# Kernel optimization log

Measured on AMD Instinct MI355X. Metric: run time of the kernel, lower is better.

Reference implementation:

```python
import jax, jax.numpy as jnp
import numpy as np

EPS = 1e-8  # torch CosineSimilarity eps


def setup_inputs() -> dict:
    key = jax.random.key(0)
    ks = jax.random.split(key, 7)
    N, D, H = 8192, 3, 256
    return {
        "pattern1": jax.random.normal(ks[0], (D,), jnp.float32),
        "pattern2": jax.random.normal(ks[1], (D,), jnp.float32),
        "working_memory": jax.random.normal(ks[2], (N, D), jnp.float32),
        "Wp": jax.random.normal(ks[3], (H, D), jnp.float32) * 0.1,
        "bp": jax.random.normal(ks[4], (H,), jnp.float32) * 0.1,
        "Wq": jax.random.normal(ks[5], (H, D), jnp.float32) * 0.1,
        "bq": jax.random.normal(ks[6], (H,), jnp.float32) * 0.1,
    }


def reference(pattern1, pattern2, working_memory, Wp, bp, Wq, bq):
    # Embed patterns and all propositions (torch Linear: x @ W.T + b)
    p1 = pattern1 @ Wp.T + bp                       # (H,)
    p2 = pattern2 @ Wp.T + bp                       # (H,)
    props = working_memory @ Wq.T + bq              # (N, H)
    prop_norm = jnp.linalg.norm(props, axis=-1)     # (N,)

    def match(pemb):
        # sigmoid(cosine_sim(pemb, props))  -> (N,)
        num = props @ pemb
        den = jnp.maximum(prop_norm * jnp.linalg.norm(pemb), EPS)
        return jax.nn.sigmoid(num / den)

    m1 = match(p1)                                  # (N,)
    m2 = match(p2)                                  # (N,)

    # Entity-link: cosine sim of scalar wm[i,2] with wm[j,0]
    obj = working_memory[:, 2]                      # (N,)
    subj = working_memory[:, 0]                     # (N,)
    num = obj[:, None] * subj[None, :]              # (N, N)
    den = jnp.maximum(jnp.abs(obj)[:, None] * jnp.abs(subj)[None, :], EPS)
    link = jax.nn.sigmoid(num / den)                # (N, N)

    out = m1[:, None] * m2[None, :] * link          # (N, N)
    N = out.shape[0]
    # zero the diagonal (i != j in the original loop)
    return out * (1.0 - jnp.eye(N, dtype=out.dtype))
```

## Files before the change

kernel.cpp:

```cpp
#include <hip/hip_runtime.h>
#include <math.h>

#define EPS 1e-8f
constexpr int N = 8192;
constexpr int ROWS_PER_BLOCK = 16;
constexpr int COLS_PER_BLOCK = 1024;
constexpr float LPOS = 0.7310585786300049f;
constexpr float LNEG = 0.2689414213699951f;

__global__ __launch_bounds__(256) void match_kernel(
    const float* __restrict__ pat1, const float* __restrict__ pat2,
    const float* __restrict__ Wp, const float* __restrict__ bp,
    const float* __restrict__ wm, const float* __restrict__ Wq,
    const float* __restrict__ bq,
    float4* __restrict__ rowpack, float* __restrict__ m2,
    float* __restrict__ subj) {
  const int row = (blockIdx.x * blockDim.x + threadIdx.x) >> 6;
  const int lane = threadIdx.x & 63;
  const float a0 = pat1[0], a1 = pat1[1], a2 = pat1[2];
  const float b0 = pat2[0], b1 = pat2[1], b2 = pat2[2];
  const float x0 = wm[row * 3 + 0];
  const float x1 = wm[row * 3 + 1];
  const float x2 = wm[row * 3 + 2];
  float s0 = 0.f, s1 = 0.f, s2 = 0.f, n1 = 0.f, n2 = 0.f;
#pragma unroll
  for (int k = 0; k < 4; ++k) {
    const int h = lane + k * 64;
    const float wp0 = Wp[h * 3 + 0], wp1 = Wp[h * 3 + 1], wp2 = Wp[h * 3 + 2];
    const float bph = bp[h];
    const float v1 = fmaf(wp0, a0, fmaf(wp1, a1, fmaf(wp2, a2, bph)));
    const float v2 = fmaf(wp0, b0, fmaf(wp1, b1, fmaf(wp2, b2, bph)));
    const float v  = fmaf(Wq[h * 3 + 0], x0,
                     fmaf(Wq[h * 3 + 1], x1,
                     fmaf(Wq[h * 3 + 2], x2, bq[h])));
    s0 = fmaf(v, v, s0);
    s1 = fmaf(v, v1, s1);
    s2 = fmaf(v, v2, s2);
    n1 = fmaf(v1, v1, n1);
    n2 = fmaf(v2, v2, n2);
  }
#pragma unroll
  for (int off = 32; off > 0; off >>= 1) {
    s0 += __shfl_xor(s0, off, 64);
    s1 += __shfl_xor(s1, off, 64);
    s2 += __shfl_xor(s2, off, 64);
    n1 += __shfl_xor(n1, off, 64);
    n2 += __shfl_xor(n2, off, 64);
  }
  if (lane == 0) {
    const float pn = sqrtf(s0);
    const float d1 = fmaxf(pn * sqrtf(n1), EPS);
    const float d2 = fmaxf(pn * sqrtf(n2), EPS);
    const float mm1 = 1.f / (1.f + __expf(-(s1 / d1)));
    const float mm2 = 1.f / (1.f + __expf(-(s2 / d2)));
    m2[row]   = mm2;
    subj[row] = x0;
    float4 rp;
    rp.x = mm1;
    rp.y = x2;
    rp.z = EPS / fabsf(x2);
    rp.w = 0.f;
    rowpack[row] = rp;
  }
}

__device__ __forceinline__ float exact_elem(float a, float oi, float m2c,
                                            float sjc) {
  const float t = oi * sjc;
  const float z = t / fmaxf(fabsf(t), EPS);
  return a * m2c * (1.f / (1.f + __expf(-z)));
}

template <bool DIAG>
__device__ __forceinline__ void run_rows(
    const float4* __restrict__ rowpack, int iBase, int jBase,
    float4 m2v, float4 sjv, float4 qp, float4 qm, float4 asj, float minasj,
    float* __restrict__ out) {
#pragma unroll
  for (int r = 0; r < ROWS_PER_BLOCK; ++r) {
    const int i = iBase + r;
    const float4 rp = rowpack[i];
    const float a = rp.x, oi = rp.y, thr = rp.z;
    const bool neg = oi < 0.f;
    float4 o;
    o.x = a * (neg ? qm.x : qp.x);
    o.y = a * (neg ? qm.y : qp.y);
    o.z = a * (neg ? qm.z : qp.z);
    o.w = a * (neg ? qm.w : qp.w);
    if (__builtin_expect(__any(minasj < thr), 0)) {
      if (asj.x < thr) o.x = exact_elem(a, oi, m2v.x, sjv.x);
      if (asj.y < thr) o.y = exact_elem(a, oi, m2v.y, sjv.y);
      if (asj.z < thr) o.z = exact_elem(a, oi, m2v.z, sjv.z);
      if (asj.w < thr) o.w = exact_elem(a, oi, m2v.w, sjv.w);
    }
    if (DIAG) {
      if (jBase + 0 == i) o.x = 0.f;
      if (jBase + 1 == i) o.y = 0.f;
      if (jBase + 2 == i) o.z = 0.f;
      if (jBase + 3 == i) o.w = 0.f;
    }
    *reinterpret_cast<float4*>(out + (size_t)i * N + jBase) = o;
  }
}

__global__ __launch_bounds__(256) void outer_kernel(
    const float4* __restrict__ rowpack, const float* __restrict__ m2,
    const float* __restrict__ subj, float* __restrict__ out) {
  const int jBase = blockIdx.x * COLS_PER_BLOCK + threadIdx.x * 4;
  const int iBase = blockIdx.y * ROWS_PER_BLOCK;
  const float4 m2v = *reinterpret_cast<const float4*>(m2 + jBase);
  const float4 sjv = *reinterpret_cast<const float4*>(subj + jBase);
  float4 qp, qm, asj;
  qp.x = m2v.x * (sjv.x > 0.f ? LPOS : LNEG);
  qp.y = m2v.y * (sjv.y > 0.f ? LPOS : LNEG);
  qp.z = m2v.z * (sjv.z > 0.f ? LPOS : LNEG);
  qp.w = m2v.w * (sjv.w > 0.f ? LPOS : LNEG);
  qm.x = m2v.x * (sjv.x > 0.f ? LNEG : LPOS);
  qm.y = m2v.y * (sjv.y > 0.f ? LNEG : LPOS);
  qm.z = m2v.z * (sjv.z > 0.f ? LNEG : LPOS);
  qm.w = m2v.w * (sjv.w > 0.f ? LNEG : LPOS);
  asj.x = fabsf(sjv.x);
  asj.y = fabsf(sjv.y);
  asj.z = fabsf(sjv.z);
  asj.w = fabsf(sjv.w);
  const float minasj = fminf(fminf(asj.x, asj.y), fminf(asj.z, asj.w));
  if ((iBase >> 10) == (int)blockIdx.x)
    run_rows<true>(rowpack, iBase, jBase, m2v, sjv, qp, qm, asj, minasj, out);
  else
    run_rows<false>(rowpack, iBase, jBase, m2v, sjv, qp, qm, asj, minasj, out);
}

extern "C" void kernel_launch(void* const* d_in, const int* in_sizes, int n_in,
                              void* d_out, int out_size, void* d_ws,
                              size_t ws_size, hipStream_t stream) {
  const float* pat1 = (const float*)d_in[0];
  const float* pat2 = (const float*)d_in[1];
  const float* wm   = (const float*)d_in[2];
  const float* Wp   = (const float*)d_in[3];
  const float* bp   = (const float*)d_in[4];
  const float* Wq   = (const float*)d_in[5];
  const float* bq   = (const float*)d_in[6];
  float* out = (float*)d_out;

  float4* rowpack = (float4*)d_ws;
  float* m2   = (float*)(rowpack + N);
  float* subj = m2 + N;

  match_kernel<<<N / 4, 256, 0, stream>>>(pat1, pat2, Wp, bp, wm, Wq, bq,
                                          rowpack, m2, subj);
  dim3 grid(N / COLS_PER_BLOCK, N / ROWS_PER_BLOCK);
  outer_kernel<<<grid, 256, 0, stream>>>(rowpack, m2, subj, out);
}
```

Measured before the change: 50.45 us.

## Make outer kernel persistent over row tiles with software-prefetched rowpack

Shrinks the outer-product grid from 8x512 to 8x64 blocks, so each block loops over 8 row tiles. It reuses the per-column setup (m2, subj, qp/qm) across all of its tiles. The rowpack entries for the next tile are prefetched into registers while the current tile is stored. This cuts per-block launch and setup overhead and hides rowpack load latency, but it raises register pressure and leaves fewer blocks in flight to saturate the store bandwidth of a 256MB write.

```diff
diff --git a/kernel.cpp b/kernel.cpp
--- a/kernel.cpp
+++ b/kernel.cpp
@@ -5,6 +5,8 @@
 constexpr int N = 8192;
 constexpr int ROWS_PER_BLOCK = 16;
 constexpr int COLS_PER_BLOCK = 1024;
+constexpr int NTILES = N / ROWS_PER_BLOCK;
+constexpr int YBLOCKS = 64;
 constexpr float LPOS = 0.7310585786300049f;
 constexpr float LNEG = 0.2689414213699951f;
 
@@ -71,43 +73,11 @@
   return a * m2c * (1.f / (1.f + __expf(-z)));
 }
 
-template <bool DIAG>
-__device__ __forceinline__ void run_rows(
-    const float4* __restrict__ rowpack, int iBase, int jBase,
-    float4 m2v, float4 sjv, float4 qp, float4 qm, float4 asj, float minasj,
-    float* __restrict__ out) {
-#pragma unroll
-  for (int r = 0; r < ROWS_PER_BLOCK; ++r) {
-    const int i = iBase + r;
-    const float4 rp = rowpack[i];
-    const float a = rp.x, oi = rp.y, thr = rp.z;
-    const bool neg = oi < 0.f;
-    float4 o;
-    o.x = a * (neg ? qm.x : qp.x);
-    o.y = a * (neg ? qm.y : qp.y);
-    o.z = a * (neg ? qm.z : qp.z);
-    o.w = a * (neg ? qm.w : qp.w);
-    if (__builtin_expect(__any(minasj < thr), 0)) {
-      if (asj.x < thr) o.x = exact_elem(a, oi, m2v.x, sjv.x);
-      if (asj.y < thr) o.y = exact_elem(a, oi, m2v.y, sjv.y);
-      if (asj.z < thr) o.z = exact_elem(a, oi, m2v.z, sjv.z);
-      if (asj.w < thr) o.w = exact_elem(a, oi, m2v.w, sjv.w);
-    }
-    if (DIAG) {
-      if (jBase + 0 == i) o.x = 0.f;
-      if (jBase + 1 == i) o.y = 0.f;
-      if (jBase + 2 == i) o.z = 0.f;
-      if (jBase + 3 == i) o.w = 0.f;
-    }
-    *reinterpret_cast<float4*>(out + (size_t)i * N + jBase) = o;
-  }
-}
-
 __global__ __launch_bounds__(256) void outer_kernel(
     const float4* __restrict__ rowpack, const float* __restrict__ m2,
     const float* __restrict__ subj, float* __restrict__ out) {
-  const int jBase = blockIdx.x * COLS_PER_BLOCK + threadIdx.x * 4;
-  const int iBase = blockIdx.y * ROWS_PER_BLOCK;
+  const int bx = blockIdx.x;
+  const int jBase = bx * COLS_PER_BLOCK + threadIdx.x * 4;
   const float4 m2v = *reinterpret_cast<const float4*>(m2 + jBase);
   const float4 sjv = *reinterpret_cast<const float4*>(subj + jBase);
   float4 qp, qm, asj;
@@ -124,10 +94,51 @@
   asj.z = fabsf(sjv.z);
   asj.w = fabsf(sjv.w);
   const float minasj = fminf(fminf(asj.x, asj.y), fminf(asj.z, asj.w));
-  if ((iBase >> 10) == (int)blockIdx.x)
-    run_rows<true>(rowpack, iBase, jBase, m2v, sjv, qp, qm, asj, minasj, out);
-  else
-    run_rows<false>(rowpack, iBase, jBase, m2v, sjv, qp, qm, asj, minasj, out);
+
+  int by = blockIdx.y;
+  float4 rp[ROWS_PER_BLOCK];
+#pragma unroll
+  for (int r = 0; r < ROWS_PER_BLOCK; ++r)
+    rp[r] = rowpack[by * ROWS_PER_BLOCK + r];
+
+  while (by < NTILES) {
+    const int nby = by + YBLOCKS;
+    float4 rpn[ROWS_PER_BLOCK];
+    if (nby < NTILES) {
+#pragma unroll
+      for (int r = 0; r < ROWS_PER_BLOCK; ++r)
+        rpn[r] = rowpack[nby * ROWS_PER_BLOCK + r];
+    }
+    const int iBase = by * ROWS_PER_BLOCK;
+    const bool diagTile = (iBase >> 10) == bx;
+#pragma unroll
+    for (int r = 0; r < ROWS_PER_BLOCK; ++r) {
+      const int i = iBase + r;
+      const float a = rp[r].x, oi = rp[r].y, thr = rp[r].z;
+      const bool neg = oi < 0.f;
+      float4 o;
+      o.x = a * (neg ? qm.x : qp.x);
+      o.y = a * (neg ? qm.y : qp.y);
+      o.z = a * (neg ? qm.z : qp.z);
+      o.w = a * (neg ? qm.w : qp.w);
+      if (__builtin_expect(__any(minasj < thr), 0)) {
+        if (asj.x < thr) o.x = exact_elem(a, oi, m2v.x, sjv.x);
+        if (asj.y < thr) o.y = exact_elem(a, oi, m2v.y, sjv.y);
+        if (asj.z < thr) o.z = exact_elem(a, oi, m2v.z, sjv.z);
+        if (asj.w < thr) o.w = exact_elem(a, oi, m2v.w, sjv.w);
+      }
+      if (diagTile) {
+        if (jBase + 0 == i) o.x = 0.f;
+        if (jBase + 1 == i) o.y = 0.f;
+        if (jBase + 2 == i) o.z = 0.f;
+        if (jBase + 3 == i) o.w = 0.f;
+      }
+      *reinterpret_cast<float4*>(out + (size_t)i * N + jBase) = o;
+    }
+#pragma unroll
+    for (int r = 0; r < ROWS_PER_BLOCK; ++r) rp[r] = rpn[r];
+    by = nby;
+  }
 }
 
 extern "C" void kernel_launch(void* const* d_in, const int* in_sizes, int n_in,
@@ -148,6 +159,6 @@
 
   match_kernel<<<N / 4, 256, 0, stream>>>(pat1, pat2, Wp, bp, wm, Wq, bq,
                                           rowpack, m2, subj);
-  dim3 grid(N / COLS_PER_BLOCK, N / ROWS_PER_BLOCK);
+  dim3 grid(N / COLS_PER_BLOCK, YBLOCKS);
   outer_kernel<<<grid, 256, 0, stream>>>(rowpack, m2, subj, out);
 }
```

Result: slower. 53.00 us (+5.1%).
